# Kernel optimization log

Hardware: AMD Instinct MI355X
Metric: run time of the kernel (lower is better)

## Reference

```python
import jax, jax.numpy as jnp
import numpy as np

D = 1024
H = 16
DK = D // H


def setup_inputs() -> dict:
    key = jax.random.key(0)
    ks = jax.random.split(key, 5)
    B, S = 4, 2048
    scale = 1.0 / np.sqrt(D)
    return {
        "inputs": jax.random.normal(ks[0], (B, S, D), dtype=jnp.float32),
        "mask": jnp.ones((B, S), dtype=jnp.int32),
        "Wq": jax.random.normal(ks[1], (D, D), dtype=jnp.float32) * scale,
        "Wk": jax.random.normal(ks[2], (D, D), dtype=jnp.float32) * scale,
        "Wv": jax.random.normal(ks[3], (D, D), dtype=jnp.float32) * scale,
        "Wo": jax.random.normal(ks[4], (D, D), dtype=jnp.float32) * scale,
    }


def reference(inputs, mask, Wq, Wk, Wv, Wo):
    B, S, _ = inputs.shape

    def split_heads(x):  # [B,S,D] -> [B,H,S,DK]
        return x.reshape(B, S, H, DK).transpose(0, 2, 1, 3)

    q = split_heads(inputs @ Wq)
    k = split_heads(inputs @ Wk)
    v = split_heads(inputs @ Wv)

    scores = jnp.einsum("bhqd,bhkd->bhqk", q, k) / jnp.sqrt(jnp.float32(DK))
    m = mask.astype(jnp.float32)[:, None, None, :]  # [B,1,1,S] over key axis
    scores = scores + (1.0 - m) * -1e9
    attn = jax.nn.softmax(scores, axis=-1)
    out = jnp.einsum("bhqk,bhkd->bhqd", attn, v)
    out = out.transpose(0, 2, 1, 3).reshape(B, S, D)
    return out @ Wo
```

## Files before the change

kernel.cpp:

```cpp
#include <hip/hip_runtime.h>
#include <hip/hip_bf16.h>
#include <stdint.h>

#define S_LEN 2048
#define D_DIM 1024
#define NH    16
#define DKH   64
#define BATCH 4

typedef __bf16 bf16x8 __attribute__((ext_vector_type(8)));
typedef float  f32x4  __attribute__((ext_vector_type(4)));

__device__ __forceinline__ unsigned short f2bf(float x) {
  unsigned u = __float_as_uint(x);
  return (unsigned short)((u + 0x7FFFu + ((u >> 16) & 1u)) >> 16);
}
__device__ __forceinline__ float bf2f(unsigned short b) {
  return __uint_as_float(((unsigned)b) << 16);
}

__device__ __forceinline__ void gll16(const void* g, void* l) {
  __builtin_amdgcn_global_load_lds((const __attribute__((address_space(1))) unsigned*)g,
                                   (__attribute__((address_space(3))) unsigned*)l, 16, 0, 0);
}

#define MFMA(a, b, c) __builtin_amdgcn_mfma_f32_16x16x32_bf16(a, b, c, 0, 0, 0)

__global__ void k_split(const float4* __restrict__ x, ushort4* __restrict__ hi,
                        ushort4* __restrict__ lo, int n4) {
  int i = blockIdx.x * 256 + threadIdx.x;
  if (i >= n4) return;
  float4 v = x[i];
  ushort4 h, l;
  h.x = f2bf(v.x); l.x = f2bf(v.x - bf2f(h.x));
  h.y = f2bf(v.y); l.y = f2bf(v.y - bf2f(h.y));
  h.z = f2bf(v.z); l.z = f2bf(v.z - bf2f(h.z));
  h.w = f2bf(v.w); l.w = f2bf(v.w - bf2f(h.w));
  hi[i] = h;
  lo[i] = l;
}

__global__ void k_wt(const float* __restrict__ W, unsigned short* __restrict__ hi,
                     unsigned short* __restrict__ lo) {
  __shared__ float t[64][65];
  const int tid = threadIdx.x;
  const int k0 = blockIdx.x * 64, n0 = blockIdx.y * 64;
#pragma unroll
  for (int i = 0; i < 16; i++) {
    int idx = i * 256 + tid;
    int r = idx >> 6, c = idx & 63;
    t[r][c] = W[(size_t)(k0 + r) * D_DIM + n0 + c];
  }
  __syncthreads();
#pragma unroll
  for (int i = 0; i < 16; i++) {
    int idx = i * 256 + tid;
    int r = idx >> 6, c = idx & 63;
    float v = t[c][r];
    unsigned short h = f2bf(v);
    size_t o = (size_t)(n0 + r) * D_DIM + k0 + c;
    hi[o] = h;
    lo[o] = f2bf(v - bf2f(h));
  }
}

template <int MODE>
__global__ __launch_bounds__(256, 2) void gemm_hilo(
    const unsigned short* __restrict__ Ahi, const unsigned short* __restrict__ Alo,
    const unsigned short* __restrict__ Bth, const unsigned short* __restrict__ Btl,
    unsigned short* __restrict__ Chi, unsigned short* __restrict__ Clo,
    float* __restrict__ Cf, float escale) {
  constexpr int N = 1024, K = 1024;
  extern __shared__ char smem[];
  char* sAh = smem;
  char* sAl = smem + 16384;
  char* sBh = smem + 32768;
  char* sBl = smem + 49152;

  const int tid = threadIdx.x;
  const int lane = tid & 63, w = tid >> 6;
  const int wr = w >> 1, wc = w & 1;
  const int m0 = blockIdx.y * 128, n0 = blockIdx.x * 128;

  int gofs[4], lofs[4];
#pragma unroll
  for (int i = 0; i < 4; i++) {
    int c = (w * 4 + i) * 64 + lane;
    int row = c >> 3, s = c & 7;
    int sp = s ^ (row & 7);
    gofs[i] = row * K + sp * 8;
    lofs[i] = (w * 4 + i) * 1024;
  }
  const unsigned short* pAh = Ahi + (size_t)m0 * K;
  const unsigned short* pAl = Alo + (size_t)m0 * K;
  const unsigned short* pBh = Bth + (size_t)n0 * K;
  const unsigned short* pBl = Btl + (size_t)n0 * K;

  f32x4 acc[4][4] = {};

  for (int kt = 0; kt < K / 64; ++kt) {
    const int ko = kt * 64;
#pragma unroll
    for (int i = 0; i < 4; i++) {
      gll16(pAh + ko + gofs[i], sAh + lofs[i]);
      gll16(pAl + ko + gofs[i], sAl + lofs[i]);
      gll16(pBh + ko + gofs[i], sBh + lofs[i]);
      gll16(pBl + ko + gofs[i], sBl + lofs[i]);
    }
    __syncthreads();
#pragma unroll
    for (int kk = 0; kk < 2; kk++) {
      bf16x8 ah[4], al[4], bh[4], bl[4];
      const int cch = kk * 4 + (lane >> 4);
#pragma unroll
      for (int mr = 0; mr < 4; mr++) {
        int row = wr * 64 + mr * 16 + (lane & 15);
        int off = row * 128 + ((cch ^ (row & 7)) << 4);
        ah[mr] = *(const bf16x8*)(sAh + off);
        al[mr] = *(const bf16x8*)(sAl + off);
      }
#pragma unroll
      for (int nr = 0; nr < 4; nr++) {
        int row = wc * 64 + nr * 16 + (lane & 15);
        int off = row * 128 + ((cch ^ (row & 7)) << 4);
        bh[nr] = *(const bf16x8*)(sBh + off);
        bl[nr] = *(const bf16x8*)(sBl + off);
      }
#pragma unroll
      for (int mr = 0; mr < 4; mr++)
#pragma unroll
        for (int nr = 0; nr < 4; nr++) {
          acc[mr][nr] = MFMA(ah[mr], bh[nr], acc[mr][nr]);
          acc[mr][nr] = MFMA(ah[mr], bl[nr], acc[mr][nr]);
          acc[mr][nr] = MFMA(al[mr], bh[nr], acc[mr][nr]);
        }
    }
    __syncthreads();
  }

#pragma unroll
  for (int mr = 0; mr < 4; mr++)
#pragma unroll
    for (int nr = 0; nr < 4; nr++)
#pragma unroll
      for (int j = 0; j < 4; j++) {
        int row = m0 + wr * 64 + mr * 16 + (lane >> 4) * 4 + j;
        int col = n0 + wc * 64 + nr * 16 + (lane & 15);
        float v = acc[mr][nr][j];
        if constexpr (MODE == 0) {
          v *= escale;
          size_t o = (size_t)row * N + col;
          unsigned short h = f2bf(v);
          Chi[o] = h;
          Clo[o] = f2bf(v - bf2f(h));
        } else if constexpr (MODE == 1) {
          int bi = row >> 11, s = row & (S_LEN - 1);
          int hh = col >> 6, d = col & (DKH - 1);
          size_t o = ((size_t)(bi * NH + hh) * DKH + d) * S_LEN + s;
          unsigned short h = f2bf(v);
          Chi[o] = h;
          Clo[o] = f2bf(v - bf2f(h));
        } else {
          Cf[(size_t)row * N + col] = v;
        }
      }
}

__global__ __launch_bounds__(256, 3) void attn3(
    const unsigned short* __restrict__ Qh, const unsigned short* __restrict__ Ql,
    const unsigned short* __restrict__ Kh, const unsigned short* __restrict__ Kl,
    const unsigned short* __restrict__ Vth, const unsigned short* __restrict__ Vtl,
    const int* __restrict__ mask,
    unsigned short* __restrict__ Oh, unsigned short* __restrict__ Ol) {
  __shared__ char sKh[8192], sKl[8192], sVh[8192], sVl[8192];
  __shared__ char sP[4][4096];

  const int tid = threadIdx.x, lane = tid & 63, w = tid >> 6;
  const int bh = blockIdx.x, b = bh >> 4, h = bh & (NH - 1);
  const int q0 = blockIdx.y * 128 + w * 32;
  const int lo16 = lane & 15, hi4 = lane >> 4;

  bf16x8 qh[2][2], ql[2][2];
#pragma unroll
  for (int g = 0; g < 2; g++)
#pragma unroll
    for (int kk = 0; kk < 2; kk++) {
      size_t base = ((size_t)(b * S_LEN + q0 + g * 16 + lo16)) * D_DIM + h * DKH + kk * 32 + hi4 * 8;
      qh[g][kk] = *(const bf16x8*)(Qh + base);
      ql[g][kk] = *(const bf16x8*)(Ql + base);
    }

  int srowK[2], scolK[2], lofs[2];
#pragma unroll
  for (int i = 0; i < 2; i++) {
    int c = (w * 2 + i) * 64 + lane;
    int row = c >> 3, s = c & 7;
    srowK[i] = row;
    scolK[i] = (s ^ (row & 7)) * 8;
    lofs[i] = c * 16 - lane * 16;
  }

  float lsum[2][4] = {};
  f32x4 oacc[2][4] = {};
  char* sPw = sP[w];

  const size_t kbase = (size_t)b * S_LEN * D_DIM + h * DKH;
  const size_t vbase = (size_t)bh * DKH * S_LEN;
  const int* mrow = mask + b * S_LEN;

  for (int sk0 = 0; sk0 < S_LEN; sk0 += 64) {
#pragma unroll
    for (int i = 0; i < 2; i++) {
      size_t gk = kbase + (size_t)(sk0 + srowK[i]) * D_DIM + scolK[i];
      gll16(Kh + gk, sKh + lofs[i]);
      gll16(Kl + gk, sKl + lofs[i]);
      size_t gv = vbase + (size_t)srowK[i] * S_LEN + sk0 + scolK[i];
      gll16(Vth + gv, sVh + lofs[i]);
      gll16(Vtl + gv, sVl + lofs[i]);
    }
    __syncthreads();

    f32x4 sc[2][4] = {};
#pragma unroll
    for (int nr = 0; nr < 4; nr++) {
      int row = nr * 16 + lo16;
      int off0 = row * 128 + (((0 * 4 + hi4) ^ (row & 7)) << 4);
      int off1 = row * 128 + (((1 * 4 + hi4) ^ (row & 7)) << 4);
      bf16x8 kh0 = *(const bf16x8*)(sKh + off0);
      bf16x8 kh1 = *(const bf16x8*)(sKh + off1);
      bf16x8 kl0 = *(const bf16x8*)(sKl + off0);
      bf16x8 kl1 = *(const bf16x8*)(sKl + off1);
#pragma unroll
      for (int g = 0; g < 2; g++) {
        sc[g][nr] = MFMA(qh[g][0], kh0, sc[g][nr]);
        sc[g][nr] = MFMA(qh[g][1], kh1, sc[g][nr]);
        sc[g][nr] = MFMA(qh[g][0], kl0, sc[g][nr]);
        sc[g][nr] = MFMA(qh[g][1], kl1, sc[g][nr]);
        sc[g][nr] = MFMA(ql[g][0], kh0, sc[g][nr]);
        sc[g][nr] = MFMA(ql[g][1], kh1, sc[g][nr]);
      }
    }

#pragma unroll
    for (int nr = 0; nr < 4; nr++) {
      float bias = mrow[sk0 + nr * 16 + lo16] ? 0.f : -1e9f;
#pragma unroll
      for (int g = 0; g < 2; g++)
#pragma unroll
        for (int j = 0; j < 4; j++) {
          float p = __expf(sc[g][nr][j] + bias);
          lsum[g][j] += p;
          int row = g * 16 + hi4 * 4 + j;
          int colb = (nr * 16 + lo16) * 2;
          *(unsigned short*)(sPw + row * 128 + (colb ^ ((row & 7) << 4))) = f2bf(p);
        }
    }

    bf16x8 pa[2][2];
#pragma unroll
    for (int g = 0; g < 2; g++)
#pragma unroll
      for (int kk = 0; kk < 2; kk++) {
        int row = g * 16 + lo16;
        int colb = kk * 64 + hi4 * 16;
        pa[g][kk] = *(const bf16x8*)(sPw + row * 128 + (colb ^ ((row & 7) << 4)));
      }

#pragma unroll
    for (int kk = 0; kk < 2; kk++)
#pragma unroll
      for (int f = 0; f < 4; f++) {
        int vrow = f * 16 + lo16;
        int voff = vrow * 128 + (((kk * 4 + hi4) ^ (vrow & 7)) << 4);
        bf16x8 vh = *(const bf16x8*)(sVh + voff);
        bf16x8 vl = *(const bf16x8*)(sVl + voff);
#pragma unroll
        for (int g = 0; g < 2; g++) {
          oacc[g][f] = MFMA(pa[g][kk], vh, oacc[g][f]);
          oacc[g][f] = MFMA(pa[g][kk], vl, oacc[g][f]);
        }
      }
    __syncthreads();
  }

  float inv[2][4];
#pragma unroll
  for (int g = 0; g < 2; g++)
#pragma unroll
    for (int j = 0; j < 4; j++) {
      float s = lsum[g][j];
      s += __shfl_xor(s, 1);
      s += __shfl_xor(s, 2);
      s += __shfl_xor(s, 4);
      s += __shfl_xor(s, 8);
      inv[g][j] = 1.f / s;
    }

#pragma unroll
  for (int g = 0; g < 2; g++)
#pragma unroll
    for (int f = 0; f < 4; f++)
#pragma unroll
      for (int j = 0; j < 4; j++) {
        int row = q0 + g * 16 + hi4 * 4 + j;
        int col = h * DKH + f * 16 + lo16;
        float v = oacc[g][f][j] * inv[g][j];
        size_t o = ((size_t)(b * S_LEN + row)) * D_DIM + col;
        unsigned short hh = f2bf(v);
        Oh[o] = hh;
        Ol[o] = f2bf(v - bf2f(hh));
      }
}

extern "C" void kernel_launch(void* const* d_in, const int* in_sizes, int n_in,
                              void* d_out, int out_size, void* d_ws, size_t ws_size,
                              hipStream_t stream) {
  const float* X = (const float*)d_in[0];
  const int* mask = (const int*)d_in[1];
  const float* Wq = (const float*)d_in[2];
  const float* Wk = (const float*)d_in[3];
  const float* Wv = (const float*)d_in[4];
  const float* Wo = (const float*)d_in[5];
  float* out = (float*)d_out;

  const size_t MB = 1024 * 1024;
  if (ws_size < 144 * MB) return;

  char* ws = (char*)d_ws;
  unsigned short* Xh = (unsigned short*)(ws);
  unsigned short* Xl = (unsigned short*)(ws + 16 * MB);
  unsigned short* Wqth = (unsigned short*)(ws + 32 * MB);
  unsigned short* Wqtl = Wqth + 1024 * 1024;
  unsigned short* Wkth = Wqtl + 1024 * 1024;
  unsigned short* Wktl = Wkth + 1024 * 1024;
  unsigned short* Wvth = Wktl + 1024 * 1024;
  unsigned short* Wvtl = Wvth + 1024 * 1024;
  unsigned short* Woth = Wvtl + 1024 * 1024;
  unsigned short* Wotl = Woth + 1024 * 1024;
  unsigned short* Qh = (unsigned short*)(ws + 48 * MB);
  unsigned short* Ql = (unsigned short*)(ws + 64 * MB);
  unsigned short* Kh = (unsigned short*)(ws + 80 * MB);
  unsigned short* Kl = (unsigned short*)(ws + 96 * MB);
  unsigned short* Vth = (unsigned short*)(ws + 112 * MB);
  unsigned short* Vtl = (unsigned short*)(ws + 128 * MB);

  const int n4 = BATCH * S_LEN * D_DIM / 4;
  k_split<<<(n4 + 255) / 256, 256, 0, stream>>>((const float4*)X, (ushort4*)Xh,
                                                (ushort4*)Xl, n4);
  dim3 wtg(16, 16);
  k_wt<<<wtg, 256, 0, stream>>>(Wq, Wqth, Wqtl);
  k_wt<<<wtg, 256, 0, stream>>>(Wk, Wkth, Wktl);
  k_wt<<<wtg, 256, 0, stream>>>(Wv, Wvth, Wvtl);
  k_wt<<<wtg, 256, 0, stream>>>(Wo, Woth, Wotl);

  dim3 gg(8, 64);
  gemm_hilo<0><<<gg, 256, 65536, stream>>>(Xh, Xl, Wqth, Wqtl, Qh, Ql, nullptr, 1.0f);
  gemm_hilo<0><<<gg, 256, 65536, stream>>>(Xh, Xl, Wkth, Wktl, Kh, Kl, nullptr, 0.125f);
  gemm_hilo<1><<<gg, 256, 65536, stream>>>(Xh, Xl, Wvth, Wvtl, Vth, Vtl, nullptr, 1.0f);

  dim3 ag(BATCH * NH, S_LEN / 128);
  attn3<<<ag, 256, 0, stream>>>(Qh, Ql, Kh, Kl, Vth, Vtl, mask, Xh, Xl);

  gemm_hilo<2><<<gg, 256, 65536, stream>>>(Xh, Xl, Woth, Wotl, nullptr, nullptr, out, 1.0f);
}
```

Before: 587.3 us.

## Double-buffer K/V tiles in attention kernel and raise MFMA wave priority

The attention kernel now keeps two LDS buffers for the K/V hi/lo tiles and prefetches the next tile with global_load_lds while computing on the current one. This is meant to hide global-load latency behind the QK and PV MFMAs. s_setprio is raised around the MFMA sections so that waves issuing matrix work are favoured. In exchange LDS use doubles and launch bounds drop from 3 to 2 blocks per CU, which reduces occupancy. The loop now has one barrier per tile.

```diff
diff --git a/kernel.cpp b/kernel.cpp
--- a/kernel.cpp
+++ b/kernel.cpp
@@ -166,13 +166,14 @@
       }
 }
 
-__global__ __launch_bounds__(256, 3) void attn3(
+__global__ __launch_bounds__(256, 2) void attn4(
     const unsigned short* __restrict__ Qh, const unsigned short* __restrict__ Ql,
     const unsigned short* __restrict__ Kh, const unsigned short* __restrict__ Kl,
     const unsigned short* __restrict__ Vth, const unsigned short* __restrict__ Vtl,
     const int* __restrict__ mask,
     unsigned short* __restrict__ Oh, unsigned short* __restrict__ Ol) {
-  __shared__ char sKh[8192], sKl[8192], sVh[8192], sVl[8192];
+  __shared__ char sKh0[8192], sKl0[8192], sVh0[8192], sVl0[8192];
+  __shared__ char sKh1[8192], sKl1[8192], sVh1[8192], sVl1[8192];
   __shared__ char sP[4][4096];
 
   const int tid = threadIdx.x, lane = tid & 63, w = tid >> 6;
@@ -208,28 +209,31 @@
   const size_t vbase = (size_t)bh * DKH * S_LEN;
   const int* mrow = mask + b * S_LEN;
 
-  for (int sk0 = 0; sk0 < S_LEN; sk0 += 64) {
+  auto STAGE = [&](char* dKh, char* dKl, char* dVh, char* dVl, int sk0) {
 #pragma unroll
     for (int i = 0; i < 2; i++) {
       size_t gk = kbase + (size_t)(sk0 + srowK[i]) * D_DIM + scolK[i];
-      gll16(Kh + gk, sKh + lofs[i]);
-      gll16(Kl + gk, sKl + lofs[i]);
+      gll16(Kh + gk, dKh + lofs[i]);
+      gll16(Kl + gk, dKl + lofs[i]);
       size_t gv = vbase + (size_t)srowK[i] * S_LEN + sk0 + scolK[i];
-      gll16(Vth + gv, sVh + lofs[i]);
-      gll16(Vtl + gv, sVl + lofs[i]);
-    }
-    __syncthreads();
-
+      gll16(Vth + gv, dVh + lofs[i]);
+      gll16(Vtl + gv, dVl + lofs[i]);
+    }
+  };
+
+  auto COMPUTE = [&](const char* cKh, const char* cKl, const char* cVh,
+                     const char* cVl, int sk0) {
     f32x4 sc[2][4] = {};
+    __builtin_amdgcn_s_setprio(1);
 #pragma unroll
     for (int nr = 0; nr < 4; nr++) {
       int row = nr * 16 + lo16;
-      int off0 = row * 128 + (((0 * 4 + hi4) ^ (row & 7)) << 4);
-      int off1 = row * 128 + (((1 * 4 + hi4) ^ (row & 7)) << 4);
-      bf16x8 kh0 = *(const bf16x8*)(sKh + off0);
-      bf16x8 kh1 = *(const bf16x8*)(sKh + off1);
-      bf16x8 kl0 = *(const bf16x8*)(sKl + off0);
-      bf16x8 kl1 = *(const bf16x8*)(sKl + off1);
+      int off0 = row * 128 + ((hi4 ^ (row & 7)) << 4);
+      int off1 = row * 128 + (((4 + hi4) ^ (row & 7)) << 4);
+      bf16x8 kh0 = *(const bf16x8*)(cKh + off0);
+      bf16x8 kh1 = *(const bf16x8*)(cKh + off1);
+      bf16x8 kl0 = *(const bf16x8*)(cKl + off0);
+      bf16x8 kl1 = *(const bf16x8*)(cKl + off1);
 #pragma unroll
       for (int g = 0; g < 2; g++) {
         sc[g][nr] = MFMA(qh[g][0], kh0, sc[g][nr]);
@@ -240,6 +244,7 @@
         sc[g][nr] = MFMA(ql[g][1], kh1, sc[g][nr]);
       }
     }
+    __builtin_amdgcn_s_setprio(0);
 
 #pragma unroll
     for (int nr = 0; nr < 4; nr++) {
@@ -266,20 +271,34 @@
         pa[g][kk] = *(const bf16x8*)(sPw + row * 128 + (colb ^ ((row & 7) << 4)));
       }
 
+    __builtin_amdgcn_s_setprio(1);
 #pragma unroll
     for (int kk = 0; kk < 2; kk++)
 #pragma unroll
       for (int f = 0; f < 4; f++) {
         int vrow = f * 16 + lo16;
         int voff = vrow * 128 + (((kk * 4 + hi4) ^ (vrow & 7)) << 4);
-        bf16x8 vh = *(const bf16x8*)(sVh + voff);
-        bf16x8 vl = *(const bf16x8*)(sVl + voff);
+        bf16x8 vh = *(const bf16x8*)(cVh + voff);
+        bf16x8 vl = *(const bf16x8*)(cVl + voff);
 #pragma unroll
         for (int g = 0; g < 2; g++) {
           oacc[g][f] = MFMA(pa[g][kk], vh, oacc[g][f]);
           oacc[g][f] = MFMA(pa[g][kk], vl, oacc[g][f]);
         }
       }
+    __builtin_amdgcn_s_setprio(0);
+  };
+
+  STAGE(sKh0, sKl0, sVh0, sVl0, 0);
+  __syncthreads();
+
+  for (int kt = 0; kt < S_LEN / 64; kt += 2) {
+    const int sk0 = kt * 64;
+    STAGE(sKh1, sKl1, sVh1, sVl1, sk0 + 64);
+    COMPUTE(sKh0, sKl0, sVh0, sVl0, sk0);
+    __syncthreads();
+    if (kt + 2 < S_LEN / 64) STAGE(sKh0, sKl0, sVh0, sVl0, sk0 + 128);
+    COMPUTE(sKh1, sKl1, sVh1, sVl1, sk0 + 64);
     __syncthreads();
   }
 
@@ -359,7 +378,7 @@
   gemm_hilo<1><<<gg, 256, 65536, stream>>>(Xh, Xl, Wvth, Wvtl, Vth, Vtl, nullptr, 1.0f);
 
   dim3 ag(BATCH * NH, S_LEN / 128);
-  attn3<<<ag, 256, 0, stream>>>(Qh, Ql, Kh, Kl, Vth, Vtl, mask, Xh, Xl);
+  attn4<<<ag, 256, 0, stream>>>(Qh, Ql, Kh, Kl, Vth, Vtl, mask, Xh, Xl);
 
   gemm_hilo<2><<<gg, 256, 65536, stream>>>(Xh, Xl, Woth, Wotl, nullptr, nullptr, out, 1.0f);
 }
```

Result: faster. 507.8 us (-13.5%).
